# Kernel optimization log

Hardware: AMD Instinct MI355X
Metric: run time of the kernel (lower is better)

The kernel has to match this reference:

```python
import jax, jax.numpy as jnp
import numpy as np

# MMTGNN (multi_head=4 branch, eval mode: dropout = identity).
# The pretrained CNN backbone is replaced by directly supplying `reps`
# (output of patches2rep reshaped to [B, T, Ns, hidden]).
# Graph is fully connected per sample (all-pairs edge_indexd incl. self
# loops), so PyG GATConv's gather/segment-softmax/scatter is expressed as
# dense per-sample attention. GATConv with edge_dim=None ignores edge_attr.
# SpectralFeatureExtractor is not defined in the source; we substitute a
# graph-weighted 2-layer MLP: W2 relu(W1 (S_thresh @ x)) using the
# thresholded cosine-similarity edge weights, matching its call signature
# and the downstream reshape(-1, hidden) + mean-pool usage.

B, T, P, H, NH, NC = 128, 8, 49, 64, 4, 2
HD = H // NH          # head_dim = 16
N = (T - 1) * P       # 343 nodes per sample (Ld = 1)
THRESH = 0.6
NEG_SLOPE = 0.2       # PyG GATConv default leaky_relu slope


def setup_inputs() -> dict:
    key = jax.random.key(0)
    ks = jax.random.split(key, 32)
    s = 0.05
    inp = {
        'reps': jax.random.normal(ks[0], (B, T, P, H), jnp.float32),
        # motion MLP: Linear(2H->H), ReLU, Linear(H->H)
        'Wm1': jax.random.normal(ks[1], (H, 2 * H)) * s,
        'bm1': jnp.zeros((H,)),
        'Wm2': jax.random.normal(ks[2], (H, H)) * s,
        'bm2': jnp.zeros((H,)),
        # GATConv 1 (heads=1): lin weight, att_src, att_dst, bias
        'Wg1': jax.random.normal(ks[3], (H, H)) * s,
        'a1s': jax.random.normal(ks[4], (H,)) * s,
        'a1d': jax.random.normal(ks[5], (H,)) * s,
        'bg1': jnp.zeros((H,)),
        # head_weight group 1: multi_head linears head_dim->head_dim
        'hw1': jax.random.normal(ks[6], (NH, HD, HD)) * s,
        'hb1': jnp.zeros((NH, HD)),
        # GATConv 2
        'Wg2': jax.random.normal(ks[7], (H, H)) * s,
        'a2s': jax.random.normal(ks[8], (H,)) * s,
        'a2d': jax.random.normal(ks[9], (H,)) * s,
        'bg2': jnp.zeros((H,)),
        # head_weight group 3
        'hw3': jax.random.normal(ks[10], (NH, HD, HD)) * s,
        'hb3': jnp.zeros((NH, HD)),
        # spectral stand-in: Linear(H->64), ReLU, Linear(64->H)
        'Ws1': jax.random.normal(ks[11], (64, H)) * s,
        'bs1': jnp.zeros((64,)),
        'Ws2': jax.random.normal(ks[12], (H, 64)) * s,
        'bs2': jnp.zeros((H,)),
        # final classifier Linear(3H -> num_classes)
        'Wf': jax.random.normal(ks[13], (NC, 3 * H)) * s,
        'bf': jnp.zeros((NC,)),
    }
    return inp


def _gat_dense(x, Wg, a_src, a_dst, bg):
    # x: [B, N, H]. Fully-connected graph incl. self loops -> dense softmax.
    xw = jnp.einsum('bnh,oh->bno', x, Wg)             # [B, N, H]
    s_src = xw @ a_src                                # [B, N]
    s_dst = xw @ a_dst                                # [B, N]
    logits = s_dst[:, :, None] + s_src[:, None, :]    # [B, N_dst, N_src]
    logits = jax.nn.leaky_relu(logits, NEG_SLOPE)
    alpha = jax.nn.softmax(logits, axis=-1)           # softmax over sources
    return jnp.einsum('bij,bjh->bih', alpha, xw) + bg


def _head_mix(x, hw, hb):
    # split features into NH chunks, per-chunk Linear, concat back
    b, n, _ = x.shape
    x4 = x.reshape(b, n, NH, HD)
    y = jnp.einsum('bnkd,ked->bnke', x4, hw) + hb     # [B, N, NH, HD]
    return y.reshape(b, n, NH * HD)


def _l2norm(x):
    # F.normalize(p=2, dim=feature), eps=1e-12
    nrm = jnp.linalg.norm(x, axis=-1, keepdims=True)
    return x / jnp.maximum(nrm, 1e-12)


def reference(reps, Wm1, bm1, Wm2, bm2,
              Wg1, a1s, a1d, bg1, hw1, hb1,
              Wg2, a2s, a2d, bg2, hw3, hb3,
              Ws1, bs1, Ws2, bs2, Wf, bf):
    b = reps.shape[0]
    F_ = T - 1
    X_f = reps[:, :F_]                                # [B, F, P, H]
    X_t = reps[:, 1:]                                 # [B, F, P, H]

    # motion node features (node index = t*P + p)
    cat = jnp.concatenate([X_f, X_t], axis=-1).reshape(b, N, 2 * H)
    node = jax.nn.relu(cat @ Wm1.T + bm1) @ Wm2.T + bm2  # [B, N, H]

    # cosine-similarity graph weights
    Xf_n = (X_f / (jnp.linalg.norm(X_f, axis=-1, keepdims=True) + 1e-4)
            ).reshape(b, N, H)
    Xt_n = (X_t / (jnp.linalg.norm(X_t, axis=-1, keepdims=True) + 1e-4)
            ).reshape(b, N, H)
    Sf = jnp.einsum('bnh,bmh->bnm', Xf_n, Xf_n)
    St = jnp.einsum('bnh,bmh->bnm', Xt_n, Xt_n)
    S = jnp.maximum(Sf, St)
    S = jnp.where(S > THRESH, S, 0.0)                 # torch.nn.Threshold

    # GAT layer 1 + multi-head mixing + l2 norm + relu
    out1 = _gat_dense(node, Wg1, a1s, a1d, bg1)
    out1 = jax.nn.relu(_l2norm(_head_mix(out1, hw1, hb1)))
    # GAT layer 2
    out2 = _gat_dense(out1, Wg2, a2s, a2d, bg2)
    out2 = jax.nn.relu(_l2norm(_head_mix(out2, hw3, hb3)))

    # spatial: mean pool per graph of concat features
    spatial = jnp.concatenate([out1, out2], axis=-1).mean(axis=1)  # [B, 2H]

    # spectral stand-in: graph-weighted aggregation + MLP, mean pool
    agg = jnp.einsum('bnm,bmh->bnh', S, node)
    sp = jax.nn.relu(agg @ Ws1.T + bs1) @ Ws2.T + bs2
    spectral = sp.mean(axis=1)                        # [B, H]

    emb = jnp.concatenate([spatial, spectral], axis=-1)  # [B, 3H]
    return emb @ Wf.T + bf                            # [B, num_classes]
```

## Files before the change

kernel.cpp:

```cpp
#include <hip/hip_runtime.h>
#include <math.h>

#define B_ 128
#define T_ 8
#define P_ 49
#define H_ 64
#define N_ 343
#define THRESH 0.6f
#define NSLOPE 0.2f

typedef float  f32x4  __attribute__((ext_vector_type(4)));
typedef short  s16x4  __attribute__((ext_vector_type(4)));
typedef short  s16x8  __attribute__((ext_vector_type(8)));
typedef unsigned short ushort_t;

#define OFF_WG2T 0
#define OFF_WM1B 8192
#define OFF_WM2B 12288
#define OFF_WG1B 16384
#define OFF_WS1B 20480
#define OFF_WS2B 24576
#define OFF_SPAT 28672
#define OFF_SPEC 45056
#define OFF_SSRC 53248
#define OFF_SDST 97152
#define OFF_SSORT 141056
#define OFF_SUFD 185088
#define OFF_PRED 229120
#define OFF_SUFE 3083008
#define OFF_PREE 5901056
#define OFF_XW   8719104
#define OFF_OUT1 11528960

__device__ __forceinline__ ushort_t f2bf(float v) {
    union { float f; unsigned int u; } c; c.f = v;
    unsigned int r = c.u + 0x7FFFu + ((c.u >> 16) & 1u);
    return (ushort_t)(r >> 16);
}
__device__ __forceinline__ s16x8 pack8(float4 a, float4 b, float s) {
    s16x8 r;
    r[0] = (short)f2bf(a.x * s); r[1] = (short)f2bf(a.y * s);
    r[2] = (short)f2bf(a.z * s); r[3] = (short)f2bf(a.w * s);
    r[4] = (short)f2bf(b.x * s); r[5] = (short)f2bf(b.y * s);
    r[6] = (short)f2bf(b.z * s); r[7] = (short)f2bf(b.w * s);
    return r;
}
__device__ __forceinline__ float dot4(float4 a) { return a.x*a.x + a.y*a.y + a.z*a.z + a.w*a.w; }

__global__ void k_prep(const float* __restrict__ Wm1, const float* __restrict__ Wm2,
                       const float* __restrict__ Wg1, const float* __restrict__ Wg2,
                       const float* __restrict__ Ws1, const float* __restrict__ Ws2,
                       float* __restrict__ Wg2T,
                       ushort_t* __restrict__ gWm1b, ushort_t* __restrict__ gWm2b,
                       ushort_t* __restrict__ gWg1b, ushort_t* __restrict__ gWs1b,
                       ushort_t* __restrict__ gWs2b) {
    int t = blockIdx.x * 256 + threadIdx.x;
    if (t < 8192) gWm1b[t] = f2bf(Wm1[t]);
    if (t < 4096) {
        int r = t >> 6, c = t & 63;
        Wg2T[c * 64 + r] = Wg2[t];
        gWm2b[t] = f2bf(Wm2[t]);
        gWg1b[t] = f2bf(Wg1[t]);
        gWs1b[t] = f2bf(Ws1[t]);
        gWs2b[t] = f2bf(Ws2[t]);
    }
}

#define CATS 136
__global__ __launch_bounds__(256) void k_node_mfma(
    const float* __restrict__ reps,
    const ushort_t* __restrict__ gWm1b, const float* __restrict__ bm1,
    const ushort_t* __restrict__ gWm2b, const float* __restrict__ bm2,
    const ushort_t* __restrict__ gWg1b, const float* __restrict__ a1s, const float* __restrict__ a1d,
    ushort_t* __restrict__ gXf16, ushort_t* __restrict__ gXt16, ushort_t* __restrict__ gNT16,
    float* __restrict__ xw, float* __restrict__ ssrc, float* __restrict__ sdst)
{
    __shared__ __align__(16) ushort_t sCat[64 * CATS];
    __shared__ __align__(16) ushort_t sW1[64 * CATS];
    __shared__ __align__(16) ushort_t sW2[64 * 72];
    __shared__ __align__(16) ushort_t sWg[64 * 72];
    __shared__ __align__(16) ushort_t hL[64 * 72];
    int tid = threadIdx.x;
    int b = blockIdx.x / 6, itile = blockIdx.x % 6;
    int i0 = itile * 64;

    for (int t = tid; t < 64 * 16; t += 256) {
        int row = t >> 4, grp = t & 15;
        *(s16x8*)&sW1[row * CATS + grp * 8] = *(const s16x8*)(gWm1b + row * 128 + grp * 8);
    }
    for (int t = tid; t < 64 * 8; t += 256) {
        int row = t >> 3, grp = t & 7;
        *(s16x8*)&sW2[row * 72 + grp * 8] = *(const s16x8*)(gWm2b + row * 64 + grp * 8);
        *(s16x8*)&sWg[row * 72 + grp * 8] = *(const s16x8*)(gWg1b + row * 64 + grp * 8);
    }
    {
        int r = tid >> 2, slice = tid & 3;
        int n = i0 + r;
        bool valid = n < N_;
        int nn = valid ? n : N_ - 1;
        int f = nn / P_, p = nn - f * P_;
        const float* xfp = reps + (((size_t)b * T_ + f) * P_ + p) * H_ + slice * 16;
        const float* xtp = xfp + P_ * H_;
        float4 f0 = ((const float4*)xfp)[0], f1 = ((const float4*)xfp)[1];
        float4 f2 = ((const float4*)xfp)[2], f3 = ((const float4*)xfp)[3];
        float4 t0 = ((const float4*)xtp)[0], t1 = ((const float4*)xtp)[1];
        float4 t2 = ((const float4*)xtp)[2], t3 = ((const float4*)xtp)[3];
        float sfs = dot4(f0) + dot4(f1) + dot4(f2) + dot4(f3);
        float sts = dot4(t0) + dot4(t1) + dot4(t2) + dot4(t3);
        sfs += __shfl_xor(sfs, 1); sfs += __shfl_xor(sfs, 2);
        sts += __shfl_xor(sts, 1); sts += __shfl_xor(sts, 2);
        float rf = 1.f / (sqrtf(sfs) + 1e-4f);
        float rt = 1.f / (sqrtf(sts) + 1e-4f);
        if (valid) {
            ushort_t* pf = gXf16 + ((size_t)b * N_ + n) * 64 + slice * 16;
            ushort_t* pt = gXt16 + ((size_t)b * N_ + n) * 64 + slice * 16;
            *(s16x8*)pf       = pack8(f0, f1, rf);
            *(s16x8*)(pf + 8) = pack8(f2, f3, rf);
            *(s16x8*)pt       = pack8(t0, t1, rt);
            *(s16x8*)(pt + 8) = pack8(t2, t3, rt);
        }
        *(s16x8*)&sCat[r * CATS + slice * 16]      = pack8(f0, f1, 1.f);
        *(s16x8*)&sCat[r * CATS + slice * 16 + 8]  = pack8(f2, f3, 1.f);
        *(s16x8*)&sCat[r * CATS + 64 + slice * 16]     = pack8(t0, t1, 1.f);
        *(s16x8*)&sCat[r * CATS + 64 + slice * 16 + 8] = pack8(t2, t3, 1.f);
    }
    __syncthreads();

    int w = tid >> 6, l = tid & 63, kg = l >> 4, m = l & 15;
    int R = w * 16;
    f32x4 acc1[4];
#pragma unroll
    for (int ht = 0; ht < 4; ++ht) acc1[ht] = (f32x4){0.f, 0.f, 0.f, 0.f};
#pragma unroll
    for (int kc = 0; kc < 4; ++kc) {
        s16x4 alo = *(const s16x4*)&sCat[(R + m) * CATS + kc * 32 + 4 * kg];
        s16x4 ahi = *(const s16x4*)&sCat[(R + m) * CATS + kc * 32 + 16 + 4 * kg];
        s16x8 av = __builtin_shufflevector(alo, ahi, 0, 1, 2, 3, 4, 5, 6, 7);
#pragma unroll
        for (int ht = 0; ht < 4; ++ht) {
            s16x4 blo = *(const s16x4*)&sW1[(ht * 16 + m) * CATS + kc * 32 + 4 * kg];
            s16x4 bhi = *(const s16x4*)&sW1[(ht * 16 + m) * CATS + kc * 32 + 16 + 4 * kg];
            s16x8 bv = __builtin_shufflevector(blo, bhi, 0, 1, 2, 3, 4, 5, 6, 7);
            acc1[ht] = __builtin_amdgcn_mfma_f32_16x16x32_bf16(av, bv, acc1[ht], 0, 0, 0);
        }
    }
#pragma unroll
    for (int ht = 0; ht < 4; ++ht) {
        float b1 = bm1[ht * 16 + m];
#pragma unroll
        for (int r = 0; r < 4; ++r)
            hL[(R + 4 * kg + r) * 72 + ht * 16 + m] = f2bf(fmaxf(acc1[ht][r] + b1, 0.f));
    }
    __syncthreads();
    f32x4 acc2[4];
#pragma unroll
    for (int ht = 0; ht < 4; ++ht) acc2[ht] = (f32x4){0.f, 0.f, 0.f, 0.f};
#pragma unroll
    for (int kc = 0; kc < 2; ++kc) {
        s16x4 alo = *(const s16x4*)&hL[(R + m) * 72 + kc * 32 + 4 * kg];
        s16x4 ahi = *(const s16x4*)&hL[(R + m) * 72 + kc * 32 + 16 + 4 * kg];
        s16x8 av = __builtin_shufflevector(alo, ahi, 0, 1, 2, 3, 4, 5, 6, 7);
#pragma unroll
        for (int ht = 0; ht < 4; ++ht) {
            s16x4 blo = *(const s16x4*)&sW2[(ht * 16 + m) * 72 + kc * 32 + 4 * kg];
            s16x4 bhi = *(const s16x4*)&sW2[(ht * 16 + m) * 72 + kc * 32 + 16 + 4 * kg];
            s16x8 bv = __builtin_shufflevector(blo, bhi, 0, 1, 2, 3, 4, 5, 6, 7);
            acc2[ht] = __builtin_amdgcn_mfma_f32_16x16x32_bf16(av, bv, acc2[ht], 0, 0, 0);
        }
    }
    __syncthreads();
#pragma unroll
    for (int ht = 0; ht < 4; ++ht) {
        float b2 = bm2[ht * 16 + m];
        int ibase = i0 + R + 4 * kg;
        ushort_t nb[4];
#pragma unroll
        for (int r = 0; r < 4; ++r) {
            nb[r] = f2bf(acc2[ht][r] + b2);
            sCat[(R + 4 * kg + r) * CATS + ht * 16 + m] = nb[r];
        }
        ushort_t* dst = gNT16 + ((size_t)b * 64 + ht * 16 + m) * 344 + ibase;
        if (ibase + 3 < N_) {
            s16x4 v; v[0] = (short)nb[0]; v[1] = (short)nb[1]; v[2] = (short)nb[2]; v[3] = (short)nb[3];
            *(s16x4*)dst = v;
        } else {
#pragma unroll
            for (int r = 0; r < 4; ++r) if (ibase + r < N_) dst[r] = nb[r];
        }
    }
    __syncthreads();
    f32x4 acc3[4];
#pragma unroll
    for (int ht = 0; ht < 4; ++ht) acc3[ht] = (f32x4){0.f, 0.f, 0.f, 0.f};
#pragma unroll
    for (int kc = 0; kc < 2; ++kc) {
        s16x4 alo = *(const s16x4*)&sCat[(R + m) * CATS + kc * 32 + 4 * kg];
        s16x4 ahi = *(const s16x4*)&sCat[(R + m) * CATS + kc * 32 + 16 + 4 * kg];
        s16x8 av = __builtin_shufflevector(alo, ahi, 0, 1, 2, 3, 4, 5, 6, 7);
#pragma unroll
        for (int ht = 0; ht < 4; ++ht) {
            s16x4 blo = *(const s16x4*)&sWg[(ht * 16 + m) * 72 + kc * 32 + 4 * kg];
            s16x4 bhi = *(const s16x4*)&sWg[(ht * 16 + m) * 72 + kc * 32 + 16 + 4 * kg];
            s16x8 bv = __builtin_shufflevector(blo, bhi, 0, 1, 2, 3, 4, 5, 6, 7);
            acc3[ht] = __builtin_amdgcn_mfma_f32_16x16x32_bf16(av, bv, acc3[ht], 0, 0, 0);
        }
    }
    float a1sv[4], a1dv[4];
#pragma unroll
    for (int ht = 0; ht < 4; ++ht) { a1sv[ht] = a1s[ht * 16 + m]; a1dv[ht] = a1d[ht * 16 + m]; }
#pragma unroll
    for (int r = 0; r < 4; ++r) {
        int i = i0 + R + 4 * kg + r;
        float sr = acc3[0][r] * a1sv[0] + acc3[1][r] * a1sv[1] + acc3[2][r] * a1sv[2] + acc3[3][r] * a1sv[3];
        float dr = acc3[0][r] * a1dv[0] + acc3[1][r] * a1dv[1] + acc3[2][r] * a1dv[2] + acc3[3][r] * a1dv[3];
        sr += __shfl_xor(sr, 1); sr += __shfl_xor(sr, 2);
        sr += __shfl_xor(sr, 4); sr += __shfl_xor(sr, 8);
        dr += __shfl_xor(dr, 1); dr += __shfl_xor(dr, 2);
        dr += __shfl_xor(dr, 4); dr += __shfl_xor(dr, 8);
        if (m == 0 && i < N_) { ssrc[b * N_ + i] = sr; sdst[b * N_ + i] = dr; }
#pragma unroll
        for (int ht = 0; ht < 4; ++ht)
            if (i < N_) xw[((size_t)b * N_ + i) * 64 + ht * 16 + m] = acc3[ht][r];
    }
}

__global__ __launch_bounds__(256, 3) void k_sim_mfma(
    const ushort_t* __restrict__ gXf, const ushort_t* __restrict__ gXt,
    const ushort_t* __restrict__ gNT,
    const ushort_t* __restrict__ gWs1b, const float* __restrict__ bs1,
    const ushort_t* __restrict__ gWs2b, const float* __restrict__ bs2,
    float* __restrict__ spec)
{
    __shared__ __align__(16) short sXf[64 * 72];
    __shared__ __align__(16) short sXt[64 * 72];
    __shared__ __align__(16) short sNT[64 * 72];
    int tid = threadIdx.x;
    int b = blockIdx.x / 6, itile = blockIdx.x % 6;
    int wv = tid >> 6, l = tid & 63;
    int kg = l >> 4, m = l & 15;
    int i0 = itile * 64;
    const ushort_t* gXfb = gXf + (size_t)b * N_ * 64;
    const ushort_t* gXtb = gXt + (size_t)b * N_ * 64;
    const ushort_t* gNTb = gNT + (size_t)b * 64 * 344;

    int ri = i0 + wv * 16 + m; if (ri > N_ - 1) ri = N_ - 1;
    s16x8 xfiB[2], xtiB[2];
#pragma unroll
    for (int c2 = 0; c2 < 2; ++c2) {
        s16x4 flo = *(const s16x4*)(gXfb + (size_t)ri * 64 + 32 * c2 + 4 * kg);
        s16x4 fhi = *(const s16x4*)(gXfb + (size_t)ri * 64 + 32 * c2 + 16 + 4 * kg);
        s16x4 tlo = *(const s16x4*)(gXtb + (size_t)ri * 64 + 32 * c2 + 4 * kg);
        s16x4 thi = *(const s16x4*)(gXtb + (size_t)ri * 64 + 32 * c2 + 16 + 4 * kg);
        xfiB[c2] = __builtin_shufflevector(flo, fhi, 0, 1, 2, 3, 4, 5, 6, 7);
        xtiB[c2] = __builtin_shufflevector(tlo, thi, 0, 1, 2, 3, 4, 5, 6, 7);
    }

    f32x4 accPV[4];
#pragma unroll
    for (int ht = 0; ht < 4; ++ht) accPV[ht] = (f32x4){0.f, 0.f, 0.f, 0.f};

#pragma unroll 1
    for (int chunk = 0; chunk < 6; ++chunk) {
        int j0 = chunk * 64;
        __syncthreads();
        for (int s = tid; s < 512; s += 256) {
            int row = s >> 3, grp = s & 7;
            int j = j0 + row;
            s16x8 vf = {0, 0, 0, 0, 0, 0, 0, 0};
            s16x8 vt = {0, 0, 0, 0, 0, 0, 0, 0};
            s16x8 vn = {0, 0, 0, 0, 0, 0, 0, 0};
            if (j < N_) {
                vf = *(const s16x8*)(gXfb + (size_t)j * 64 + grp * 8);
                vt = *(const s16x8*)(gXtb + (size_t)j * 64 + grp * 8);
            }
            if (j0 + grp * 8 + 8 <= 344)
                vn = *(const s16x8*)(gNTb + (size_t)row * 344 + j0 + grp * 8);
            *(s16x8*)(&sXf[row * 72 + grp * 8]) = vf;
            *(s16x8*)(&sXt[row * 72 + grp * 8]) = vt;
            *(s16x8*)(&sNT[row * 72 + grp * 8]) = vn;
        }
        __syncthreads();
        int npair = (chunk == 5) ? 1 : 2;
#pragma unroll 1
        for (int pr = 0; pr < npair; ++pr) {
            s16x8 pa;
#pragma unroll
            for (int sub = 0; sub < 2; ++sub) {
                int arow = (pr * 2 + sub) * 16 + m;
                f32x4 sf = (f32x4){0.f, 0.f, 0.f, 0.f};
                f32x4 st = (f32x4){0.f, 0.f, 0.f, 0.f};
#pragma unroll
                for (int hc = 0; hc < 2; ++hc) {
                    int h0 = hc * 32;
                    s16x4 alo = *(const s16x4*)(&sXf[arow * 72 + h0 + 4 * kg]);
                    s16x4 ahi = *(const s16x4*)(&sXf[arow * 72 + h0 + 16 + 4 * kg]);
                    s16x8 av = __builtin_shufflevector(alo, ahi, 0, 1, 2, 3, 4, 5, 6, 7);
                    sf = __builtin_amdgcn_mfma_f32_16x16x32_bf16(av, xfiB[hc], sf, 0, 0, 0);
                    s16x4 blo = *(const s16x4*)(&sXt[arow * 72 + h0 + 4 * kg]);
                    s16x4 bhi = *(const s16x4*)(&sXt[arow * 72 + h0 + 16 + 4 * kg]);
                    s16x8 bv = __builtin_shufflevector(blo, bhi, 0, 1, 2, 3, 4, 5, 6, 7);
                    st = __builtin_amdgcn_mfma_f32_16x16x32_bf16(bv, xtiB[hc], st, 0, 0, 0);
                }
#pragma unroll
                for (int r = 0; r < 4; ++r) {
                    float v = fmaxf(sf[r], st[r]);
                    v = (v > THRESH) ? v : 0.f;
                    pa[sub * 4 + r] = (short)f2bf(v);
                }
            }
            int jl0 = pr * 32;
#pragma unroll
            for (int ht = 0; ht < 4; ++ht) {
                s16x4 nlo = *(const s16x4*)(&sNT[(ht * 16 + m) * 72 + jl0 + 4 * kg]);
                s16x4 nhi = *(const s16x4*)(&sNT[(ht * 16 + m) * 72 + jl0 + 16 + 4 * kg]);
                s16x8 nv = __builtin_shufflevector(nlo, nhi, 0, 1, 2, 3, 4, 5, 6, 7);
                accPV[ht] = __builtin_amdgcn_mfma_f32_16x16x32_bf16(pa, nv, accPV[ht], 0, 0, 0);
            }
        }
    }
    __syncthreads();
    for (int t = tid; t < 64 * 8; t += 256) {
        int row = t >> 3, grp = t & 7;
        *(s16x8*)&sXt[row * 72 + grp * 8] = *(const s16x8*)(gWs1b + row * 64 + grp * 8);
    }
    int R = wv * 16;
#pragma unroll
    for (int ht = 0; ht < 4; ++ht)
#pragma unroll
        for (int r = 0; r < 4; ++r)
            sXf[(R + 4 * kg + r) * 72 + ht * 16 + m] = (short)f2bf(accPV[ht][r]);
    __syncthreads();
    f32x4 h4[4];
#pragma unroll
    for (int ht = 0; ht < 4; ++ht) h4[ht] = (f32x4){0.f, 0.f, 0.f, 0.f};
#pragma unroll
    for (int kc = 0; kc < 2; ++kc) {
        s16x4 alo = *(const s16x4*)&sXf[(R + m) * 72 + kc * 32 + 4 * kg];
        s16x4 ahi = *(const s16x4*)&sXf[(R + m) * 72 + kc * 32 + 16 + 4 * kg];
        s16x8 av = __builtin_shufflevector(alo, ahi, 0, 1, 2, 3, 4, 5, 6, 7);
#pragma unroll
        for (int ht = 0; ht < 4; ++ht) {
            s16x4 blo = *(const s16x4*)&sXt[(ht * 16 + m) * 72 + kc * 32 + 4 * kg];
            s16x4 bhi = *(const s16x4*)&sXt[(ht * 16 + m) * 72 + kc * 32 + 16 + 4 * kg];
            s16x8 bv = __builtin_shufflevector(blo, bhi, 0, 1, 2, 3, 4, 5, 6, 7);
            h4[ht] = __builtin_amdgcn_mfma_f32_16x16x32_bf16(av, bv, h4[ht], 0, 0, 0);
        }
    }
#pragma unroll
    for (int ht = 0; ht < 4; ++ht) {
        float b1 = bs1[ht * 16 + m];
#pragma unroll
        for (int r = 0; r < 4; ++r)
            sNT[(R + 4 * kg + r) * 72 + ht * 16 + m] = (short)f2bf(fmaxf(h4[ht][r] + b1, 0.f));
    }
    __syncthreads();
    for (int t = tid; t < 64 * 8; t += 256) {
        int row = t >> 3, grp = t & 7;
        *(s16x8*)&sXt[row * 72 + grp * 8] = *(const s16x8*)(gWs2b + row * 64 + grp * 8);
    }
    __syncthreads();
    f32x4 sp4[4];
#pragma unroll
    for (int ht = 0; ht < 4; ++ht) sp4[ht] = (f32x4){0.f, 0.f, 0.f, 0.f};
#pragma unroll
    for (int kc = 0; kc < 2; ++kc) {
        s16x4 alo = *(const s16x4*)&sNT[(R + m) * 72 + kc * 32 + 4 * kg];
        s16x4 ahi = *(const s16x4*)&sNT[(R + m) * 72 + kc * 32 + 16 + 4 * kg];
        s16x8 av = __builtin_shufflevector(alo, ahi, 0, 1, 2, 3, 4, 5, 6, 7);
#pragma unroll
        for (int ht = 0; ht < 4; ++ht) {
            s16x4 blo = *(const s16x4*)&sXt[(ht * 16 + m) * 72 + kc * 32 + 4 * kg];
            s16x4 bhi = *(const s16x4*)&sXt[(ht * 16 + m) * 72 + kc * 32 + 16 + 4 * kg];
            s16x8 bv = __builtin_shufflevector(blo, bhi, 0, 1, 2, 3, 4, 5, 6, 7);
            sp4[ht] = __builtin_amdgcn_mfma_f32_16x16x32_bf16(av, bv, sp4[ht], 0, 0, 0);
        }
    }
#pragma unroll
    for (int ht = 0; ht < 4; ++ht) {
        float b2 = bs2[ht * 16 + m];
        float s = 0.f;
#pragma unroll
        for (int r = 0; r < 4; ++r) {
            int i = i0 + R + 4 * kg + r;
            s += (i < N_) ? (sp4[ht][r] + b2) : 0.f;
        }
        s += __shfl_xor(s, 16); s += __shfl_xor(s, 32);
        if (l < 16) atomicAdd(&spec[b * 64 + ht * 16 + m], s);
    }
}

#define NSEG 16
#define SEGSZ 22
__global__ __launch_bounds__(1024) void k_sortscan(
    const float* __restrict__ ssrc, const float* __restrict__ xw,
    float* __restrict__ ssort, float* __restrict__ SufE, float* __restrict__ PreE,
    float* __restrict__ SufD, float* __restrict__ PreD)
{
    __shared__ float sv[512];
    __shared__ int   si[512];
    __shared__ float w1L[344], w2L[344];
    __shared__ float segT[NSEG * 64];
    __shared__ float segD[NSEG];
    int tid = threadIdx.x, b = blockIdx.x;
    for (int q = tid; q < 512; q += 1024) {
        sv[q] = (q < N_) ? ssrc[b * N_ + q] : 3.0e38f;
        si[q] = q;
    }
    __syncthreads();
    for (int k = 2; k <= 512; k <<= 1)
        for (int j = k >> 1; j > 0; j >>= 1) {
            for (int e = tid; e < 512; e += 1024) {
                int l = e ^ j;
                if (l > e) {
                    float a = sv[e], c = sv[l];
                    bool up = ((e & k) == 0);
                    if (up ? (a > c) : (a < c)) {
                        sv[e] = c; sv[l] = a;
                        int t = si[e]; si[e] = si[l]; si[l] = t;
                    }
                }
            }
            __syncthreads();
        }
    if (tid < N_) {
        float v = sv[tid];
        w1L[tid] = __expf(v);
        w2L[tid] = __expf(0.2f * v);
        ssort[(size_t)b * 344 + tid] = v;
    }
    __syncthreads();
    int t = tid >> 6, h = tid & 63;
    int qs = t * SEGSZ, qe = min(qs + SEGSZ, N_);
    const float* xwb = xw + (size_t)b * N_ * 64;
    size_t base = (size_t)b * 344;
    float r = 0.f, rd = 0.f;
    for (int q = qe - 1; q >= qs; --q) {
        float w = w1L[q];
        r += w * xwb[(size_t)si[q] * 64 + h];
        rd += w;
    }
    segT[t * 64 + h] = r; if (h == 0) segD[t] = rd;
    __syncthreads();
    float bsum = 0.f, bden = 0.f;
    for (int t2 = t + 1; t2 < NSEG; ++t2) { bsum += segT[t2 * 64 + h]; bden += segD[t2]; }
    r = bsum; rd = bden;
    for (int q = qe - 1; q >= qs; --q) {
        float w = w1L[q];
        r += w * xwb[(size_t)si[q] * 64 + h];
        rd += w;
        SufE[(base + q) * 64 + h] = r;
        if (h == 0) SufD[base + q] = rd;
    }
    if (t == 0) { SufE[(base + 343) * 64 + h] = 0.f; if (h == 0) SufD[base + 343] = 0.f; }
    __syncthreads();
    r = 0.f; rd = 0.f;
    for (int q = qs; q < qe; ++q) {
        float w = w2L[q];
        r += w * xwb[(size_t)si[q] * 64 + h];
        rd += w;
    }
    segT[t * 64 + h] = r; if (h == 0) segD[t] = rd;
    __syncthreads();
    bsum = 0.f; bden = 0.f;
    for (int t2 = 0; t2 < t; ++t2) { bsum += segT[t2 * 64 + h]; bden += segD[t2]; }
    r = bsum; rd = bden;
    for (int q = qs; q < qe; ++q) {
        PreE[(base + q) * 64 + h] = r;
        if (h == 0) PreD[base + q] = rd;
        float w = w2L[q];
        r += w * xwb[(size_t)si[q] * 64 + h];
        rd += w;
    }
    if (t == NSEG - 1) { PreE[(base + 343) * 64 + h] = r; if (h == 0) PreD[base + 343] = rd; }
}

#define GSEG 8
#define GROWS 43
template <int FUSE_XW>
__global__ __launch_bounds__(256) void k_gatfuse(
    const float* __restrict__ sdst, const float* __restrict__ ssort,
    const float* __restrict__ SufE, const float* __restrict__ PreE,
    const float* __restrict__ SufD, const float* __restrict__ PreD,
    const float* __restrict__ bg, const float* __restrict__ hw, const float* __restrict__ hb,
    const float* __restrict__ WgT, const float* __restrict__ as_, const float* __restrict__ ad_,
    float* __restrict__ xw2, float* __restrict__ ssrc2, float* __restrict__ sdst2,
    float* __restrict__ spatial, int soff)
{
    __shared__ float sW[4096];
    __shared__ float xs[4][64];
    __shared__ float accL[4][64];
    __shared__ float ssL[344];
    int tid = threadIdx.x, wv = tid >> 6, ln = tid & 63;
    int b = blockIdx.x >> 3, seg = blockIdx.x & 7;
    if (FUSE_XW)
        for (int t = tid; t < 1024; t += 256) ((float4*)sW)[t] = ((const float4*)WgT)[t];
    for (int t = tid; t < N_; t += 256) ssL[t] = ssort[(size_t)b * 344 + t];
    __syncthreads();
    int start = seg * GROWS, end = min(start + GROWS, N_);
    float bgv = bg[ln], hbv = hb[ln];
    int k = ln >> 4;
    float asv = 0.f, adv = 0.f;
    if (FUSE_XW) { asv = as_[ln]; adv = ad_[ln]; }
    float hwr[16];
#pragma unroll
    for (int d = 0; d < 16; ++d) hwr[d] = hw[ln * 16 + d];
    float spacc = 0.f;
    for (int i = start + wv; i < end; i += 4) {
        int idx = b * N_ + i;
        float di = sdst[idx];
        float key = -di;
        int lo = 0, hi = N_;
        while (lo < hi) { int mid = (lo + hi) >> 1; if (ssL[mid] >= key) hi = mid; else lo = mid + 1; }
        int p = lo;
        float ed = __expf(di), e2 = __expf(0.2f * di);
        size_t base = (size_t)b * 344 + p;
        float acc = ed * SufE[base * 64 + ln] + e2 * PreE[base * 64 + ln];
        float den = ed * SufD[base] + e2 * PreD[base];
        float g = acc / den + bgv;
        float y = hbv;
#pragma unroll
        for (int d = 0; d < 16; ++d) y += hwr[d] * __shfl(g, (k << 4) | d);
        float ssum = y * y;
#pragma unroll
        for (int s = 1; s < 64; s <<= 1) ssum += __shfl_xor(ssum, s);
        float rr = 1.f / fmaxf(sqrtf(ssum), 1e-12f);
        y = fmaxf(y * rr, 0.f);
        spacc += y;
        if (FUSE_XW) {
            xs[wv][ln] = y;
            float a0 = 0.f, a1 = 0.f, a2 = 0.f, a3 = 0.f;
#pragma unroll 4
            for (int h = 0; h < 64; h += 4) {
                a0 += xs[wv][h]     * sW[h * 64 + ln];
                a1 += xs[wv][h + 1] * sW[(h + 1) * 64 + ln];
                a2 += xs[wv][h + 2] * sW[(h + 2) * 64 + ln];
                a3 += xs[wv][h + 3] * sW[(h + 3) * 64 + ln];
            }
            float a = (a0 + a1) + (a2 + a3);
            xw2[(size_t)idx * 64 + ln] = a;
            float ps = a * asv, pd = a * adv;
#pragma unroll
            for (int s = 1; s < 64; s <<= 1) { ps += __shfl_xor(ps, s); pd += __shfl_xor(pd, s); }
            if (ln == 0) { ssrc2[idx] = ps; sdst2[idx] = pd; }
        }
    }
    accL[wv][ln] = spacc;
    __syncthreads();
    if (wv == 0) {
        float s = accL[0][ln] + accL[1][ln] + accL[2][ln] + accL[3][ln];
        atomicAdd(&spatial[b * 128 + soff + ln], s);
    }
}

__global__ void k_final(const float* __restrict__ spatial, const float* __restrict__ spectral,
                        const float* __restrict__ Wf, const float* __restrict__ bf_,
                        float* __restrict__ out)
{
    int b = blockIdx.x, ln = threadIdx.x;
    float inv = 1.f / (float)N_;
    float e0 = spatial[b * 128 + ln] * inv;
    float e1 = spatial[b * 128 + 64 + ln] * inv;
    float e2 = spectral[b * 64 + ln] * inv;
#pragma unroll
    for (int c = 0; c < 2; c++) {
        float a = e0 * Wf[c * 192 + ln] + e1 * Wf[c * 192 + 64 + ln] + e2 * Wf[c * 192 + 128 + ln];
#pragma unroll
        for (int s = 1; s < 64; s <<= 1) a += __shfl_xor(a, s);
        if (ln == 0) out[b * 2 + c] = a + bf_[c];
    }
}

extern "C" void kernel_launch(void* const* d_in, const int* in_sizes, int n_in,
                              void* d_out, int out_size, void* d_ws, size_t ws_size,
                              hipStream_t stream)
{
    const float* reps = (const float*)d_in[0];
    const float* Wm1  = (const float*)d_in[1];
    const float* bm1  = (const float*)d_in[2];
    const float* Wm2  = (const float*)d_in[3];
    const float* bm2  = (const float*)d_in[4];
    const float* Wg1  = (const float*)d_in[5];
    const float* a1s  = (const float*)d_in[6];
    const float* a1d  = (const float*)d_in[7];
    const float* bg1  = (const float*)d_in[8];
    const float* hw1  = (const float*)d_in[9];
    const float* hb1  = (const float*)d_in[10];
    const float* Wg2  = (const float*)d_in[11];
    const float* a2s  = (const float*)d_in[12];
    const float* a2d  = (const float*)d_in[13];
    const float* bg2  = (const float*)d_in[14];
    const float* hw3  = (const float*)d_in[15];
    const float* hb3  = (const float*)d_in[16];
    const float* Ws1  = (const float*)d_in[17];
    const float* bs1  = (const float*)d_in[18];
    const float* Ws2  = (const float*)d_in[19];
    const float* bs2  = (const float*)d_in[20];
    const float* Wf   = (const float*)d_in[21];
    const float* bf_  = (const float*)d_in[22];

    float* ws = (float*)d_ws;
    float* Wg2T = ws + OFF_WG2T;
    ushort_t* gWm1b = (ushort_t*)(ws + OFF_WM1B);
    ushort_t* gWm2b = (ushort_t*)(ws + OFF_WM2B);
    ushort_t* gWg1b = (ushort_t*)(ws + OFF_WG1B);
    ushort_t* gWs1b = (ushort_t*)(ws + OFF_WS1B);
    ushort_t* gWs2b = (ushort_t*)(ws + OFF_WS2B);
    float* spat = ws + OFF_SPAT;
    float* spec = ws + OFF_SPEC;
    float* ssrc = ws + OFF_SSRC;
    float* sdst = ws + OFF_SDST;
    float* ssort= ws + OFF_SSORT;
    float* SufD = ws + OFF_SUFD;
    float* PreD = ws + OFF_PRED;
    float* SufE = ws + OFF_SUFE;
    float* PreE = ws + OFF_PREE;
    float* xwb  = ws + OFF_XW;
    ushort_t* gXf16 = (ushort_t*)(ws + OFF_SUFE);
    ushort_t* gXt16 = (ushort_t*)(ws + OFF_PREE);
    ushort_t* gNT16 = (ushort_t*)(ws + OFF_OUT1);

    hipMemsetAsync(spat, 0, (16384 + 8192) * sizeof(float), stream);
    k_prep<<<32, 256, 0, stream>>>(Wm1, Wm2, Wg1, Wg2, Ws1, Ws2,
                                   Wg2T, gWm1b, gWm2b, gWg1b, gWs1b, gWs2b);
    k_node_mfma<<<B_ * 6, 256, 0, stream>>>(reps, gWm1b, bm1, gWm2b, bm2,
                                            gWg1b, a1s, a1d,
                                            gXf16, gXt16, gNT16, xwb, ssrc, sdst);
    k_sim_mfma<<<B_ * 6, 256, 0, stream>>>(gXf16, gXt16, gNT16,
                                           gWs1b, bs1, gWs2b, bs2, spec);
    k_sortscan<<<B_, 1024, 0, stream>>>(ssrc, xwb, ssort, SufE, PreE, SufD, PreD);
    k_gatfuse<1><<<B_ * GSEG, 256, 0, stream>>>(sdst, ssort, SufE, PreE, SufD, PreD,
                                                bg1, hw1, hb1, Wg2T, a2s, a2d,
                                                xwb, ssrc, sdst, spat, 0);
    k_sortscan<<<B_, 1024, 0, stream>>>(ssrc, xwb, ssort, SufE, PreE, SufD, PreD);
    k_gatfuse<0><<<B_ * GSEG, 256, 0, stream>>>(sdst, ssort, SufE, PreE, SufD, PreD,
                                                bg2, hw3, hb3, nullptr, nullptr, nullptr,
                                                nullptr, nullptr, nullptr, spat, 64);
    k_final<<<B_, 64, 0, stream>>>(spat, spec, Wf, bf_, (float*)d_out);
}
```

Baseline: 287.8 us.

## Split sortscan suffix/prefix across blocks, halve gatfuse segments, precompute row search

The sortscan kernel now launches two blocks per sample, one building the exp(s) suffix sums and the other the exp(0.2 s) prefix sums, so the two scans run in parallel instead of one after the other. The cost is a duplicated bitonic sort per block. The GAT fuse kernel uses 16 segments of 22 rows instead of 8 of 43, giving more blocks but loading the shared weights more times. Its per-row binary search, exponentials and denominator reciprocal are done once per row by separate threads up front, taking them out of the serial per-warp loop.

```diff
diff --git a/kernel.cpp b/kernel.cpp
--- a/kernel.cpp
+++ b/kernel.cpp
@@ -398,10 +398,11 @@
 {
     __shared__ float sv[512];
     __shared__ int   si[512];
-    __shared__ float w1L[344], w2L[344];
+    __shared__ float wL[344];
     __shared__ float segT[NSEG * 64];
     __shared__ float segD[NSEG];
-    int tid = threadIdx.x, b = blockIdx.x;
+    int tid = threadIdx.x;
+    int b = blockIdx.x >> 1, dir = blockIdx.x & 1;
     for (int q = tid; q < 512; q += 1024) {
         sv[q] = (q < N_) ? ssrc[b * N_ + q] : 3.0e38f;
         si[q] = q;
@@ -424,58 +425,59 @@
         }
     if (tid < N_) {
         float v = sv[tid];
-        w1L[tid] = __expf(v);
-        w2L[tid] = __expf(0.2f * v);
-        ssort[(size_t)b * 344 + tid] = v;
+        wL[tid] = dir ? __expf(0.2f * v) : __expf(v);
+        if (!dir) ssort[(size_t)b * 344 + tid] = v;
     }
     __syncthreads();
     int t = tid >> 6, h = tid & 63;
     int qs = t * SEGSZ, qe = min(qs + SEGSZ, N_);
     const float* xwb = xw + (size_t)b * N_ * 64;
     size_t base = (size_t)b * 344;
-    float r = 0.f, rd = 0.f;
-    for (int q = qe - 1; q >= qs; --q) {
-        float w = w1L[q];
-        r += w * xwb[(size_t)si[q] * 64 + h];
-        rd += w;
-    }
-    segT[t * 64 + h] = r; if (h == 0) segD[t] = rd;
-    __syncthreads();
-    float bsum = 0.f, bden = 0.f;
-    for (int t2 = t + 1; t2 < NSEG; ++t2) { bsum += segT[t2 * 64 + h]; bden += segD[t2]; }
-    r = bsum; rd = bden;
-    for (int q = qe - 1; q >= qs; --q) {
-        float w = w1L[q];
-        r += w * xwb[(size_t)si[q] * 64 + h];
-        rd += w;
-        SufE[(base + q) * 64 + h] = r;
-        if (h == 0) SufD[base + q] = rd;
-    }
-    if (t == 0) { SufE[(base + 343) * 64 + h] = 0.f; if (h == 0) SufD[base + 343] = 0.f; }
-    __syncthreads();
-    r = 0.f; rd = 0.f;
-    for (int q = qs; q < qe; ++q) {
-        float w = w2L[q];
-        r += w * xwb[(size_t)si[q] * 64 + h];
-        rd += w;
-    }
-    segT[t * 64 + h] = r; if (h == 0) segD[t] = rd;
-    __syncthreads();
-    bsum = 0.f; bden = 0.f;
-    for (int t2 = 0; t2 < t; ++t2) { bsum += segT[t2 * 64 + h]; bden += segD[t2]; }
-    r = bsum; rd = bden;
-    for (int q = qs; q < qe; ++q) {
-        PreE[(base + q) * 64 + h] = r;
-        if (h == 0) PreD[base + q] = rd;
-        float w = w2L[q];
-        r += w * xwb[(size_t)si[q] * 64 + h];
-        rd += w;
-    }
-    if (t == NSEG - 1) { PreE[(base + 343) * 64 + h] = r; if (h == 0) PreD[base + 343] = rd; }
-}
-
-#define GSEG 8
-#define GROWS 43
+    if (dir == 0) {
+        float r = 0.f, rd = 0.f;
+        for (int q = qe - 1; q >= qs; --q) {
+            float w = wL[q];
+            r += w * xwb[(size_t)si[q] * 64 + h];
+            rd += w;
+        }
+        segT[t * 64 + h] = r; if (h == 0) segD[t] = rd;
+        __syncthreads();
+        float bsum = 0.f, bden = 0.f;
+        for (int t2 = t + 1; t2 < NSEG; ++t2) { bsum += segT[t2 * 64 + h]; bden += segD[t2]; }
+        r = bsum; rd = bden;
+        for (int q = qe - 1; q >= qs; --q) {
+            float w = wL[q];
+            r += w * xwb[(size_t)si[q] * 64 + h];
+            rd += w;
+            SufE[(base + q) * 64 + h] = r;
+            if (h == 0) SufD[base + q] = rd;
+        }
+        if (t == 0) { SufE[(base + 343) * 64 + h] = 0.f; if (h == 0) SufD[base + 343] = 0.f; }
+    } else {
+        float r = 0.f, rd = 0.f;
+        for (int q = qs; q < qe; ++q) {
+            float w = wL[q];
+            r += w * xwb[(size_t)si[q] * 64 + h];
+            rd += w;
+        }
+        segT[t * 64 + h] = r; if (h == 0) segD[t] = rd;
+        __syncthreads();
+        float bsum = 0.f, bden = 0.f;
+        for (int t2 = 0; t2 < t; ++t2) { bsum += segT[t2 * 64 + h]; bden += segD[t2]; }
+        r = bsum; rd = bden;
+        for (int q = qs; q < qe; ++q) {
+            PreE[(base + q) * 64 + h] = r;
+            if (h == 0) PreD[base + q] = rd;
+            float w = wL[q];
+            r += w * xwb[(size_t)si[q] * 64 + h];
+            rd += w;
+        }
+        if (t == NSEG - 1) { PreE[(base + 343) * 64 + h] = r; if (h == 0) PreD[base + 343] = rd; }
+    }
+}
+
+#define GSEG 16
+#define GROWS 22
 template <int FUSE_XW>
 __global__ __launch_bounds__(256) void k_gatfuse(
     const float* __restrict__ sdst, const float* __restrict__ ssort,
@@ -490,13 +492,27 @@
     __shared__ float xs[4][64];
     __shared__ float accL[4][64];
     __shared__ float ssL[344];
+    __shared__ float pEd[GROWS], pE2[GROWS], pInv[GROWS];
+    __shared__ int   pP[GROWS];
     int tid = threadIdx.x, wv = tid >> 6, ln = tid & 63;
-    int b = blockIdx.x >> 3, seg = blockIdx.x & 7;
+    int b = blockIdx.x >> 4, seg = blockIdx.x & 15;
     if (FUSE_XW)
         for (int t = tid; t < 1024; t += 256) ((float4*)sW)[t] = ((const float4*)WgT)[t];
     for (int t = tid; t < N_; t += 256) ssL[t] = ssort[(size_t)b * 344 + t];
     __syncthreads();
     int start = seg * GROWS, end = min(start + GROWS, N_);
+    int cnt = end - start;
+    if (tid < cnt) {
+        float di = sdst[b * N_ + start + tid];
+        float key = -di;
+        int lo = 0, hi = N_;
+        while (lo < hi) { int mid = (lo + hi) >> 1; if (ssL[mid] >= key) hi = mid; else lo = mid + 1; }
+        float ed = __expf(di), e2 = __expf(0.2f * di);
+        size_t base = (size_t)b * 344 + lo;
+        float den = ed * SufD[base] + e2 * PreD[base];
+        pP[tid] = lo; pEd[tid] = ed; pE2[tid] = e2; pInv[tid] = 1.f / den;
+    }
+    __syncthreads();
     float bgv = bg[ln], hbv = hb[ln];
     int k = ln >> 4;
     float asv = 0.f, adv = 0.f;
@@ -505,18 +521,12 @@
 #pragma unroll
     for (int d = 0; d < 16; ++d) hwr[d] = hw[ln * 16 + d];
     float spacc = 0.f;
-    for (int i = start + wv; i < end; i += 4) {
+    for (int r = wv; r < cnt; r += 4) {
+        int i = start + r;
         int idx = b * N_ + i;
-        float di = sdst[idx];
-        float key = -di;
-        int lo = 0, hi = N_;
-        while (lo < hi) { int mid = (lo + hi) >> 1; if (ssL[mid] >= key) hi = mid; else lo = mid + 1; }
-        int p = lo;
-        float ed = __expf(di), e2 = __expf(0.2f * di);
-        size_t base = (size_t)b * 344 + p;
-        float acc = ed * SufE[base * 64 + ln] + e2 * PreE[base * 64 + ln];
-        float den = ed * SufD[base] + e2 * PreD[base];
-        float g = acc / den + bgv;
+        float ed = pEd[r], e2 = pE2[r], inv = pInv[r];
+        size_t base = (size_t)b * 344 + pP[r];
+        float g = (ed * SufE[base * 64 + ln] + e2 * PreE[base * 64 + ln]) * inv + bgv;
         float y = hbv;
 #pragma unroll
         for (int d = 0; d < 16; ++d) y += hwr[d] * __shfl(g, (k << 4) | d);
@@ -627,11 +637,11 @@
                                             gXf16, gXt16, gNT16, xwb, ssrc, sdst);
     k_sim_mfma<<<B_ * 6, 256, 0, stream>>>(gXf16, gXt16, gNT16,
                                            gWs1b, bs1, gWs2b, bs2, spec);
-    k_sortscan<<<B_, 1024, 0, stream>>>(ssrc, xwb, ssort, SufE, PreE, SufD, PreD);
+    k_sortscan<<<B_ * 2, 1024, 0, stream>>>(ssrc, xwb, ssort, SufE, PreE, SufD, PreD);
     k_gatfuse<1><<<B_ * GSEG, 256, 0, stream>>>(sdst, ssort, SufE, PreE, SufD, PreD,
                                                 bg1, hw1, hb1, Wg2T, a2s, a2d,
                                                 xwb, ssrc, sdst, spat, 0);
-    k_sortscan<<<B_, 1024, 0, stream>>>(ssrc, xwb, ssort, SufE, PreE, SufD, PreD);
+    k_sortscan<<<B_ * 2, 1024, 0, stream>>>(ssrc, xwb, ssort, SufE, PreE, SufD, PreD);
     k_gatfuse<0><<<B_ * GSEG, 256, 0, stream>>>(sdst, ssort, SufE, PreE, SufD, PreD,
                                                 bg2, hw3, hb3, nullptr, nullptr, nullptr,
                                                 nullptr, nullptr, nullptr, spat, 64);
```

After: 262.9 us. 8.6% less time.
